# Optimization experiments

Hardware: AMD Instinct MI355X
Metric: run time of the kernel (lower is better)

The kernel has to match this reference:

```python
import jax, jax.numpy as jnp
import numpy as np

B, LP, LQ, H = 8, 2048, 2048, 1024


def setup_inputs() -> dict:
    key = jax.random.key(0)
    k1, k2, k3, k4, k5 = jax.random.split(key, 5)
    proj_p = jax.random.normal(k1, (B, LP, H), dtype=jnp.float32)
    proj_q = jax.random.normal(k2, (B, LQ, H), dtype=jnp.float32)
    seq_len = jax.random.randint(k3, (B,), 1, LQ + 1)  # valid key lengths in [1, LQ]
    bound = 1.0 / np.sqrt(H)
    W_t = jax.random.uniform(k4, (H, H), minval=-bound, maxval=bound, dtype=jnp.float32)
    b_t = jax.random.uniform(k5, (H,), minval=-bound, maxval=bound, dtype=jnp.float32)
    return {"proj_p": proj_p, "proj_q": proj_q, "W_t": W_t, "b_t": b_t, "seq_len": seq_len}


def reference(proj_p, proj_q, W_t, b_t, seq_len):
    # trans_q = Linear(proj_q): [B, LQ, H]
    trans_q = jnp.einsum('bqh,oh->bqo', proj_q, W_t) + b_t
    # att_weights = proj_p @ trans_q^T : [B, LP, LQ]
    scores = jnp.einsum('bph,bqh->bpq', proj_p, trans_q)
    # mask over the key dim per seq_len (mask-multiply, softmax, re-mask, renorm)
    mask = (jnp.arange(LQ)[None, None, :] < seq_len[:, None, None]).astype(scores.dtype)
    att = jax.nn.softmax(scores * mask, axis=-1) * mask
    att = att / (jnp.sum(att, axis=-1, keepdims=True) + 1e-13)
    # att_vec = att_norm @ proj_q : [B, LP, H]
    return jnp.einsum('bpq,bqh->bph', att, proj_q)
```

## Files before the change

kernel.cpp:

```cpp
#include <hip/hip_runtime.h>
#include <stdint.h>

#define NB 8
#define LP 2048
#define LQS 2048
#define HD 1024

typedef _Float16 h16;
typedef _Float16 half8 __attribute__((ext_vector_type(8)));
typedef _Float16 half4 __attribute__((ext_vector_type(4)));
typedef float f32x4 __attribute__((ext_vector_type(4)));

__device__ __forceinline__ void gload16(const void* g, void* l) {
    __builtin_amdgcn_global_load_lds(
        (const __attribute__((address_space(1))) void*)g,
        (__attribute__((address_space(3))) void*)l, 16, 0, 0);
}

__global__ __launch_bounds__(256) void cast_split(const float* __restrict__ src,
                                                  h16* __restrict__ hi,
                                                  h16* __restrict__ lo, long n) {
    long stride = (long)gridDim.x * 256 * 4;
    for (long i = ((long)blockIdx.x * 256 + threadIdx.x) * 4; i < n; i += stride) {
        f32x4 v = *(const f32x4*)(src + i);
        half4 h, l;
#pragma unroll
        for (int j = 0; j < 4; ++j) {
            h16 hh = (h16)v[j];
            h[j] = hh;
            l[j] = (h16)(v[j] - (float)hh);
        }
        *(half4*)(hi + i) = h;
        *(half4*)(lo + i) = l;
    }
}

__global__ __launch_bounds__(256) void transpose_v(const h16* __restrict__ Q16,
                                                   h16* __restrict__ VT) {
    int b = blockIdx.z, q0 = blockIdx.y * 64, h0 = blockIdx.x * 64;
    __shared__ h16 tile[64][72];
    const h16* src = Q16 + ((size_t)b * LQS + q0) * HD + h0;
    int t = threadIdx.x;
    for (int c = t; c < 512; c += 256) {
        int row = c >> 3, col = (c & 7) * 8;
        *(half8*)&tile[row][col] = *(const half8*)(src + (size_t)row * HD + col);
    }
    __syncthreads();
    h16* dst = VT + ((size_t)b * HD + h0) * LQS + q0;
    for (int c = t; c < 512; c += 256) {
        int hh = c >> 3, q8 = (c & 7) * 8;
        half8 v;
#pragma unroll
        for (int j = 0; j < 8; ++j) v[j] = tile[q8 + j][hh];
        *(half8*)(dst + (size_t)hh * LQS + q8) = v;
    }
}

__device__ __forceinline__ void gemm128(const h16* __restrict__ A0, int lda,
                                        const h16* __restrict__ B0, int ldb,
                                        int Kdim, f32x4 acc[4][4],
                                        h16* ldsA, h16* ldsB) {
    const int t = threadIdx.x;
    const int lane = t & 63, wave = t >> 6;
    const int wr = wave >> 1, wc = wave & 1;
    const int fr = lane & 15, fq = lane >> 4;

    for (int kt = 0; kt < Kdim; kt += 64) {
        __syncthreads();
#pragma unroll
        for (int i = 0; i < 4; ++i) {
            int c = i * 256 + t;
            int row = c >> 3, j = c & 7;
            int sc = j ^ (row & 7);
            gload16(A0 + (size_t)row * lda + kt + sc * 8,
                    ldsA + (size_t)(i * 256 + wave * 64) * 8);
            gload16(B0 + (size_t)row * ldb + kt + sc * 8,
                    ldsB + (size_t)(i * 256 + wave * 64) * 8);
        }
        asm volatile("s_waitcnt vmcnt(0)" ::: "memory");
        __syncthreads();
#pragma unroll
        for (int kk = 0; kk < 2; ++kk) {
            half8 av[4], bv[4];
#pragma unroll
            for (int m = 0; m < 4; ++m) {
                int row = wr * 64 + m * 16 + fr;
                int ch = (kk * 4 + fq) ^ (row & 7);
                av[m] = *(const half8*)(ldsA + row * 64 + ch * 8);
            }
#pragma unroll
            for (int n = 0; n < 4; ++n) {
                int row = wc * 64 + n * 16 + fr;
                int ch = (kk * 4 + fq) ^ (row & 7);
                bv[n] = *(const half8*)(ldsB + row * 64 + ch * 8);
            }
#pragma unroll
            for (int m = 0; m < 4; ++m)
#pragma unroll
                for (int n = 0; n < 4; ++n)
                    acc[m][n] = __builtin_amdgcn_mfma_f32_16x16x32_f16(av[m], bv[n], acc[m][n], 0, 0, 0);
        }
    }
}

#define ACC_INIT(acc) \
    f32x4 acc[4][4];  \
    _Pragma("unroll") for (int m_ = 0; m_ < 4; ++m_) _Pragma("unroll") for (int n_ = 0; n_ < 4; ++n_) acc[m_][n_] = (f32x4){0.f, 0.f, 0.f, 0.f};

__global__ __launch_bounds__(256) void k_transq(const h16* __restrict__ Qhi,
                                                const h16* __restrict__ Qlo,
                                                const h16* __restrict__ Whi,
                                                const h16* __restrict__ Wlo,
                                                const float* __restrict__ bias,
                                                const int* __restrict__ seq,
                                                h16* __restrict__ Khi,
                                                h16* __restrict__ Klo) {
    int nt = blockIdx.x, mt = blockIdx.y;
    int b = mt >> 4;
    int q0 = (mt & 15) * 128;
    if (q0 >= seq[b]) return;
    __shared__ h16 ldsA[128 * 64], ldsB[128 * 64];
    ACC_INIT(acc);
    size_t aoff = (size_t)mt * 128 * HD;
    const h16* Bh = Whi + (size_t)nt * 128 * HD;
    const h16* Bl = Wlo + (size_t)nt * 128 * HD;
    gemm128(Qhi + aoff, HD, Bh, HD, HD, acc, ldsA, ldsB);
    gemm128(Qhi + aoff, HD, Bl, HD, HD, acc, ldsA, ldsB);
    gemm128(Qlo + aoff, HD, Bh, HD, HD, acc, ldsA, ldsB);
    int lane = threadIdx.x & 63, wave = threadIdx.x >> 6;
    int wr = wave >> 1, wc = wave & 1, fr = lane & 15, fq = lane >> 4;
    size_t rowbase = (size_t)mt * 128;
#pragma unroll
    for (int m = 0; m < 4; ++m)
#pragma unroll
        for (int n = 0; n < 4; ++n) {
            int col = nt * 128 + wc * 64 + n * 16 + fr;
            float bv = bias[col];
#pragma unroll
            for (int j = 0; j < 4; ++j) {
                int row = wr * 64 + m * 16 + fq * 4 + j;
                float tv = acc[m][n][j] + bv;
                h16 th = (h16)tv;
                size_t idx = (rowbase + row) * HD + col;
                Khi[idx] = th;
                Klo[idx] = (h16)(tv - (float)th);
            }
        }
}

__global__ __launch_bounds__(256) void k_scores(const h16* __restrict__ Phi,
                                                const h16* __restrict__ Plo,
                                                const h16* __restrict__ Khi,
                                                const h16* __restrict__ Klo,
                                                const int* __restrict__ seq,
                                                float* __restrict__ S, int b0) {
    int qt = blockIdx.x, pt = blockIdx.y, lb = blockIdx.z;
    int b = b0 + lb;
    if (qt * 128 >= seq[b]) return;
    __shared__ h16 ldsA[128 * 64], ldsB[128 * 64];
    ACC_INIT(acc);
    size_t aoff = ((size_t)b * LP + pt * 128) * HD;
    size_t boff = ((size_t)b * LQS + qt * 128) * HD;
    gemm128(Phi + aoff, HD, Khi + boff, HD, HD, acc, ldsA, ldsB);
    gemm128(Phi + aoff, HD, Klo + boff, HD, HD, acc, ldsA, ldsB);
    gemm128(Plo + aoff, HD, Khi + boff, HD, HD, acc, ldsA, ldsB);
    int lane = threadIdx.x & 63, wave = threadIdx.x >> 6;
    int wr = wave >> 1, wc = wave & 1, fr = lane & 15, fq = lane >> 4;
    float* C = S + ((size_t)lb * LP + pt * 128) * LQS + qt * 128;
#pragma unroll
    for (int m = 0; m < 4; ++m)
#pragma unroll
        for (int n = 0; n < 4; ++n)
#pragma unroll
            for (int j = 0; j < 4; ++j) {
                int row = wr * 64 + m * 16 + fq * 4 + j;
                int col = wc * 64 + n * 16 + fr;
                C[(size_t)row * LQS + col] = acc[m][n][j];
            }
}

__global__ __launch_bounds__(256) void softmax_k(float* __restrict__ S,
                                                 const int* __restrict__ seq, int b0) {
    int wid = threadIdx.x >> 6, lane = threadIdx.x & 63;
    int r = blockIdx.x * 4 + wid;
    int b = b0 + (r >> 11);
    int L = seq[b];
    const float* Srow = S + (size_t)r * LQS;
    h16* Prow = (h16*)(S + (size_t)r * LQS);
    float m = -INFINITY;
    for (int i = lane; i < L; i += 64) m = fmaxf(m, Srow[i]);
#pragma unroll
    for (int off = 32; off; off >>= 1) m = fmaxf(m, __shfl_xor(m, off));
    float M = (L < LQS) ? fmaxf(m, 0.f) : m;
    float s = 0.f;
    for (int i = lane; i < L; i += 64) s += expf(Srow[i] - M);
#pragma unroll
    for (int off = 32; off; off >>= 1) s += __shfl_xor(s, off);
    float corr = (L < LQS) ? (float)(LQS - L) * expf(-M) : 0.f;
    float denom = s + 1e-13f * (s + corr);
    float inv = 1.f / denom;
    int Lpad = (L + 63) & ~63;
    for (int i = lane; i < L; i += 64) {
        float e = expf(Srow[i] - M) * inv;
        Prow[i] = (h16)e;
    }
    for (int i = L + lane; i < Lpad; i += 64) Prow[i] = (h16)0.f;
}

__global__ __launch_bounds__(256) void k_pv(const h16* __restrict__ PA,
                                            const h16* __restrict__ VT,
                                            const int* __restrict__ seq,
                                            float* __restrict__ out, int b0) {
    int ht = blockIdx.x, pt = blockIdx.y, lb = blockIdx.z;
    int b = b0 + lb;
    int L = seq[b];
    int Lpad = (L + 63) & ~63;
    __shared__ h16 ldsA[128 * 64], ldsB[128 * 64];
    ACC_INIT(acc);
    const h16* A0 = PA + ((size_t)lb * LP + pt * 128) * (2 * LQS);
    const h16* B0 = VT + ((size_t)b * HD + ht * 128) * LQS;
    gemm128(A0, 2 * LQS, B0, LQS, Lpad, acc, ldsA, ldsB);
    int lane = threadIdx.x & 63, wave = threadIdx.x >> 6;
    int wr = wave >> 1, wc = wave & 1, fr = lane & 15, fq = lane >> 4;
    float* C = out + ((size_t)b * LP + pt * 128) * HD + ht * 128;
#pragma unroll
    for (int m = 0; m < 4; ++m)
#pragma unroll
        for (int n = 0; n < 4; ++n)
#pragma unroll
            for (int j = 0; j < 4; ++j) {
                int row = wr * 64 + m * 16 + fq * 4 + j;
                int col = wc * 64 + n * 16 + fr;
                C[(size_t)row * HD + col] = acc[m][n][j];
            }
}

extern "C" void kernel_launch(void* const* d_in, const int* in_sizes, int n_in,
                              void* d_out, int out_size, void* d_ws, size_t ws_size,
                              hipStream_t stream) {
    const float* proj_p = (const float*)d_in[0];
    const float* proj_q = (const float*)d_in[1];
    const float* W_t    = (const float*)d_in[2];
    const float* b_t    = (const float*)d_in[3];
    const int*   seq    = (const int*)d_in[4];
    float* out = (float*)d_out;

    char* ws = (char*)d_ws;
    const size_t MB = (size_t)1 << 20;
    h16*  Qhi = (h16*)(ws + 0 * MB);
    h16*  Qlo = (h16*)(ws + 32 * MB);
    h16*  Khi = (h16*)(ws + 64 * MB);
    h16*  Klo = (h16*)(ws + 96 * MB);
    h16*  Plo = (h16*)(ws + 128 * MB);
    float* S  = (float*)(ws + 160 * MB);
    h16*  Whi = (h16*)(ws + 160 * MB);
    h16*  Wlo = (h16*)(ws + 162 * MB);
    h16*  Phi = Qhi;
    h16*  VT  = Qlo;
    const h16* PA = (const h16*)S;
    (void)in_sizes; (void)n_in; (void)out_size;

    int cb = 8;
    if (ws_size > 0) {
        size_t avail = (ws_size > 160 * MB) ? (ws_size - 160 * MB) : 0;
        int fit = (int)(avail / (16 * MB));
        cb = (fit >= 8) ? 8 : (fit >= 4) ? 4 : (fit >= 2) ? 2 : 1;
    }

    cast_split<<<1024, 256, 0, stream>>>(W_t, Whi, Wlo, (long)HD * HD);
    cast_split<<<4096, 256, 0, stream>>>(proj_q, Qhi, Qlo, (long)NB * LQS * HD);
    k_transq<<<dim3(HD / 128, NB * LQS / 128), 256, 0, stream>>>(Qhi, Qlo, Whi, Wlo, b_t, seq, Khi, Klo);
    transpose_v<<<dim3(HD / 64, LQS / 64, NB), 256, 0, stream>>>(Qhi, VT);
    cast_split<<<4096, 256, 0, stream>>>(proj_p, Phi, Plo, (long)NB * LP * HD);
    for (int b0 = 0; b0 < NB; b0 += cb) {
        k_scores<<<dim3(LQS / 128, LP / 128, cb), 256, 0, stream>>>(Phi, Plo, Khi, Klo, seq, S, b0);
        softmax_k<<<cb * LP / 4, 256, 0, stream>>>(S, seq, b0);
        k_pv<<<dim3(HD / 128, LP / 128, cb), 256, 0, stream>>>(PA, VT, seq, out, b0);
    }
}
```

Before: 649.0 us.

## Fuse split-precision GEMM passes into one K loop and swizzle blocks across XCDs

The three separate hi/lo GEMM passes in the linear and score kernels become a single K loop that stages all four hi/lo tiles in LDS and issues three MFMAs per fragment pair. This removes two of the three reloads of each operand and the associated barriers. LDS use per block doubles to 64KB, which may lower occupancy and raise register pressure from holding four fragment sets. A block-index swizzle that groups neighbouring tiles onto the same XCD is also added to the linear, score and PV kernels to improve L2 reuse.

Result: faster. 524.5 us (-19.2%).

```diff
diff --git a/kernel.cpp b/kernel.cpp
--- a/kernel.cpp
+++ b/kernel.cpp
@@ -15,6 +15,15 @@
     __builtin_amdgcn_global_load_lds(
         (const __attribute__((address_space(1))) void*)g,
         (__attribute__((address_space(3))) void*)l, 16, 0, 0);
+}
+
+__device__ __forceinline__ void xcd_swz(int& bx, int& by) {
+    int gx = gridDim.x;
+    int orig = blockIdx.x + gx * blockIdx.y;
+    int nw8 = (gx * gridDim.y) >> 3;
+    int swz = (orig & 7) * nw8 + (orig >> 3);
+    bx = swz % gx;
+    by = swz / gx;
 }
 
 __global__ __launch_bounds__(256) void cast_split(const float* __restrict__ src,
@@ -56,6 +65,63 @@
     }
 }
 
+#define STAGE_TILE(SRC, LD, LDS_)                                   \
+    _Pragma("unroll") for (int i_ = 0; i_ < 4; ++i_) {              \
+        int c_ = i_ * 256 + t;                                      \
+        int row_ = c_ >> 3, j_ = c_ & 7;                            \
+        int sc_ = j_ ^ (row_ & 7);                                  \
+        gload16((SRC) + (size_t)row_ * (LD) + kt + sc_ * 8,         \
+                (LDS_) + (size_t)(i_ * 256 + wave * 64) * 8);       \
+    }
+
+__device__ __forceinline__ void gemm_split(const h16* __restrict__ Ah,
+                                           const h16* __restrict__ Al, int lda,
+                                           const h16* __restrict__ Bh,
+                                           const h16* __restrict__ Bl, int ldb,
+                                           int Kdim, f32x4 acc[4][4],
+                                           h16* lAh, h16* lAl, h16* lBh, h16* lBl) {
+    const int t = threadIdx.x;
+    const int lane = t & 63, wave = t >> 6;
+    const int wr = wave >> 1, wc = wave & 1;
+    const int fr = lane & 15, fq = lane >> 4;
+
+    for (int kt = 0; kt < Kdim; kt += 64) {
+        __syncthreads();
+        STAGE_TILE(Ah, lda, lAh);
+        STAGE_TILE(Al, lda, lAl);
+        STAGE_TILE(Bh, ldb, lBh);
+        STAGE_TILE(Bl, ldb, lBl);
+        asm volatile("s_waitcnt vmcnt(0)" ::: "memory");
+        __syncthreads();
+#pragma unroll
+        for (int kk = 0; kk < 2; ++kk) {
+            half8 ah[4], al[4], bh[4], bl[4];
+#pragma unroll
+            for (int m = 0; m < 4; ++m) {
+                int row = wr * 64 + m * 16 + fr;
+                int ch = (kk * 4 + fq) ^ (row & 7);
+                ah[m] = *(const half8*)(lAh + row * 64 + ch * 8);
+                al[m] = *(const half8*)(lAl + row * 64 + ch * 8);
+            }
+#pragma unroll
+            for (int n = 0; n < 4; ++n) {
+                int row = wc * 64 + n * 16 + fr;
+                int ch = (kk * 4 + fq) ^ (row & 7);
+                bh[n] = *(const half8*)(lBh + row * 64 + ch * 8);
+                bl[n] = *(const half8*)(lBl + row * 64 + ch * 8);
+            }
+#pragma unroll
+            for (int m = 0; m < 4; ++m)
+#pragma unroll
+                for (int n = 0; n < 4; ++n) {
+                    acc[m][n] = __builtin_amdgcn_mfma_f32_16x16x32_f16(ah[m], bh[n], acc[m][n], 0, 0, 0);
+                    acc[m][n] = __builtin_amdgcn_mfma_f32_16x16x32_f16(ah[m], bl[n], acc[m][n], 0, 0, 0);
+                    acc[m][n] = __builtin_amdgcn_mfma_f32_16x16x32_f16(al[m], bh[n], acc[m][n], 0, 0, 0);
+                }
+        }
+    }
+}
+
 __device__ __forceinline__ void gemm128(const h16* __restrict__ A0, int lda,
                                         const h16* __restrict__ B0, int ldb,
                                         int Kdim, f32x4 acc[4][4],
@@ -67,16 +133,8 @@
 
     for (int kt = 0; kt < Kdim; kt += 64) {
         __syncthreads();
-#pragma unroll
-        for (int i = 0; i < 4; ++i) {
-            int c = i * 256 + t;
-            int row = c >> 3, j = c & 7;
-            int sc = j ^ (row & 7);
-            gload16(A0 + (size_t)row * lda + kt + sc * 8,
-                    ldsA + (size_t)(i * 256 + wave * 64) * 8);
-            gload16(B0 + (size_t)row * ldb + kt + sc * 8,
-                    ldsB + (size_t)(i * 256 + wave * 64) * 8);
-        }
+        STAGE_TILE(A0, lda, ldsA);
+        STAGE_TILE(B0, ldb, ldsB);
         asm volatile("s_waitcnt vmcnt(0)" ::: "memory");
         __syncthreads();
 #pragma unroll
@@ -115,18 +173,17 @@
                                                 const int* __restrict__ seq,
                                                 h16* __restrict__ Khi,
                                                 h16* __restrict__ Klo) {
-    int nt = blockIdx.x, mt = blockIdx.y;
+    int nt, mt;
+    xcd_swz(nt, mt);
     int b = mt >> 4;
     int q0 = (mt & 15) * 128;
     if (q0 >= seq[b]) return;
-    __shared__ h16 ldsA[128 * 64], ldsB[128 * 64];
+    __shared__ h16 lAh[128 * 64], lAl[128 * 64], lBh[128 * 64], lBl[128 * 64];
     ACC_INIT(acc);
     size_t aoff = (size_t)mt * 128 * HD;
-    const h16* Bh = Whi + (size_t)nt * 128 * HD;
-    const h16* Bl = Wlo + (size_t)nt * 128 * HD;
-    gemm128(Qhi + aoff, HD, Bh, HD, HD, acc, ldsA, ldsB);
-    gemm128(Qhi + aoff, HD, Bl, HD, HD, acc, ldsA, ldsB);
-    gemm128(Qlo + aoff, HD, Bh, HD, HD, acc, ldsA, ldsB);
+    size_t boff = (size_t)nt * 128 * HD;
+    gemm_split(Qhi + aoff, Qlo + aoff, HD, Whi + boff, Wlo + boff, HD, HD, acc,
+               lAh, lAl, lBh, lBl);
     int lane = threadIdx.x & 63, wave = threadIdx.x >> 6;
     int wr = wave >> 1, wc = wave & 1, fr = lane & 15, fq = lane >> 4;
     size_t rowbase = (size_t)mt * 128;
@@ -154,16 +211,17 @@
                                                 const h16* __restrict__ Klo,
                                                 const int* __restrict__ seq,
                                                 float* __restrict__ S, int b0) {
-    int qt = blockIdx.x, pt = blockIdx.y, lb = blockIdx.z;
+    int qt, pt;
+    xcd_swz(qt, pt);
+    int lb = blockIdx.z;
     int b = b0 + lb;
     if (qt * 128 >= seq[b]) return;
-    __shared__ h16 ldsA[128 * 64], ldsB[128 * 64];
+    __shared__ h16 lAh[128 * 64], lAl[128 * 64], lBh[128 * 64], lBl[128 * 64];
     ACC_INIT(acc);
     size_t aoff = ((size_t)b * LP + pt * 128) * HD;
     size_t boff = ((size_t)b * LQS + qt * 128) * HD;
-    gemm128(Phi + aoff, HD, Khi + boff, HD, HD, acc, ldsA, ldsB);
-    gemm128(Phi + aoff, HD, Klo + boff, HD, HD, acc, ldsA, ldsB);
-    gemm128(Plo + aoff, HD, Khi + boff, HD, HD, acc, ldsA, ldsB);
+    gemm_split(Phi + aoff, Plo + aoff, HD, Khi + boff, Klo + boff, HD, HD, acc,
+               lAh, lAl, lBh, lBl);
     int lane = threadIdx.x & 63, wave = threadIdx.x >> 6;
     int wr = wave >> 1, wc = wave & 1, fr = lane & 15, fq = lane >> 4;
     float* C = S + ((size_t)lb * LP + pt * 128) * LQS + qt * 128;
@@ -211,7 +269,9 @@
                                             const h16* __restrict__ VT,
                                             const int* __restrict__ seq,
                                             float* __restrict__ out, int b0) {
-    int ht = blockIdx.x, pt = blockIdx.y, lb = blockIdx.z;
+    int ht, pt;
+    xcd_swz(ht, pt);
+    int lb = blockIdx.z;
     int b = b0 + lb;
     int L = seq[b];
     int Lpad = (L + 63) & ~63;
```
